# Kernel tuning notes

Hardware: AMD Instinct MI355X
Metric: run time of the kernel (lower is better)

The kernel has to match this reference:

```python
import jax, jax.numpy as jnp
import numpy as np

D = 12  # grid size per axis (self.shape = [12,12,12])
BN_EPS = 1e-5


def _scatter(feats, idx, B):
    # feats: [N, C], idx: [N, 4] = (b, z, y, x). Coords are unique -> .set is exact.
    g = jnp.zeros((B, D, D, D, feats.shape[-1]), feats.dtype)
    return g.at[idx[:, 0], idx[:, 1], idx[:, 2], idx[:, 3]].set(feats)


def _subm_conv_bn_relu(feats, idx, B, W, b, gamma, beta):
    # Submanifold 3x3x3 conv == dense SAME conv on zero-filled grid, restricted
    # to the active sites (inactive neighbors contribute zero features).
    g = _scatter(feats, idx, B)  # [B, D, D, D, Cin]
    y = jax.lax.conv_general_dilated(
        g, W, window_strides=(1, 1, 1), padding='SAME',
        dimension_numbers=('NDHWC', 'DHWIO', 'NDHWC')) + b
    f = y[idx[:, 0], idx[:, 1], idx[:, 2], idx[:, 3]]  # gather active -> [N, Cout]
    # BatchNorm1d (training mode): biased batch stats over the N active points.
    mu = f.mean(axis=0)
    var = f.var(axis=0)
    f = (f - mu) * jax.lax.rsqrt(var + BN_EPS) * gamma + beta
    return jax.nn.relu(f)


def setup_inputs() -> dict:
    key = jax.random.key(0)
    B, per, Cin = 512, 864, 16
    N = B * per
    k_feat, k_coord, kp = jax.random.split(key, 3)
    # unique active voxels per batch element
    pkeys = jax.random.split(k_coord, B)
    lin = jax.vmap(lambda k: jax.random.permutation(k, D * D * D))(pkeys)[:, :per]  # [B, per]
    z, y, x = lin // (D * D), (lin // D) % D, lin % D
    bids = jnp.broadcast_to(jnp.arange(B)[:, None], (B, per))
    indices = jnp.stack([bids, z, y, x], axis=-1).reshape(N, 4).astype(jnp.int32)
    features = jax.random.normal(k_feat, (N, Cin), dtype=jnp.float32)
    ks = jax.random.split(kp, 6)
    inp = {
        'features': features, 'indices': indices, 'batch_size': B,
        'W0': jax.random.normal(ks[0], (3, 3, 3, Cin, 64), jnp.float32) * 0.05,
        'b0': jax.random.normal(ks[1], (64,), jnp.float32) * 0.05,
        'gamma0': jnp.ones((64,), jnp.float32), 'beta0': jnp.zeros((64,), jnp.float32),
        'W1': jax.random.normal(ks[2], (3, 3, 3, 64, 128), jnp.float32) * 0.05,
        'b1': jax.random.normal(ks[3], (128,), jnp.float32) * 0.05,
        'gamma1': jnp.ones((128,), jnp.float32), 'beta1': jnp.zeros((128,), jnp.float32),
        'W2': jax.random.normal(ks[4], (3, 3, 3, 128, 64), jnp.float32) * 0.05,
        'b2': jax.random.normal(ks[5], (64,), jnp.float32) * 0.05,
        'gamma2': jnp.ones((64,), jnp.float32), 'beta2': jnp.zeros((64,), jnp.float32),
    }
    return inp


def reference(features, indices, batch_size, W0, b0, gamma0, beta0,
              W1, b1, gamma1, beta1, W2, b2, gamma2, beta2):
    B = int(batch_size)
    f = _subm_conv_bn_relu(features, indices, B, W0, b0, gamma0, beta0)
    f = _subm_conv_bn_relu(f, indices, B, W1, b1, gamma1, beta1)
    f = _subm_conv_bn_relu(f, indices, B, W2, b2, gamma2, beta2)
    g = _scatter(f, indices, B)                 # [B, D, D, D, Cout]
    return jnp.transpose(g, (0, 4, 1, 2, 3))    # spconv .dense(): [B, C, D, H, W]
```

## Files before the change

### kernel.cpp

```cpp
#include <hip/hip_runtime.h>

#define DD 12
#define VOX 1728
#define BN_EPS 1e-5f
#define BATCH 512
#define PER 864
#define PERZ 865

typedef __attribute__((ext_vector_type(8))) short short8;
typedef __attribute__((ext_vector_type(4))) float f32x4;
typedef unsigned short u16;

__device__ inline u16 f2b(float f) {
    union { float f; unsigned u; } v; v.f = f;
    unsigned r = v.u + 0x7fffu + ((v.u >> 16) & 1u);
    return (u16)(r >> 16);
}
__device__ inline float b2f(u16 h) {
    union { unsigned u; float f; } v; v.u = ((unsigned)h) << 16;
    return v.f;
}
constexpr int ilog2(int v) { return v == 1 ? 0 : 1 + ilog2(v / 2); }

__device__ __forceinline__ void async_copy16(const void* g, void* l) {
    __builtin_amdgcn_global_load_lds(
        (const __attribute__((address_space(1))) void*)g,
        (__attribute__((address_space(3))) void*)l, 16, 0, 0);
}

template<int N> __device__ __forceinline__ void wait_vm() {
    if constexpr (N == 0)       asm volatile("s_waitcnt vmcnt(0)"  ::: "memory");
    else if constexpr (N == 8)  asm volatile("s_waitcnt vmcnt(8)"  ::: "memory");
    else if constexpr (N == 10) asm volatile("s_waitcnt vmcnt(10)" ::: "memory");
    else if constexpr (N == 12) asm volatile("s_waitcnt vmcnt(12)" ::: "memory");
    else if constexpr (N == 18) asm volatile("s_waitcnt vmcnt(18)" ::: "memory");
    else static_assert(N == 0, "unhandled vmcnt value");
}

__global__ void build_map_kernel(const int* __restrict__ idx, int* __restrict__ map, int N) {
    int p = blockIdx.x * blockDim.x + threadIdx.x;
    if (p >= N) return;
    const int4 v = ((const int4*)idx)[p];
    map[v.x * VOX + (v.y * DD + v.z) * DD + v.w] = p;
}

__global__ void build_nbr_kernel(const int* __restrict__ idx, const int* __restrict__ map,
                                 u16* __restrict__ nbr, int N) {
    int t = blockIdx.x * blockDim.x + threadIdx.x;
    int p = t >> 5, nk = t & 31;
    if (p >= N) return;
    u16 out = PER;
    if (nk < 27) {
        const int4 v = ((const int4*)idx)[p];
        int dz = nk / 9 - 1, dy = (nk / 3) % 3 - 1, dx = nk % 3 - 1;
        int zz = v.y + dz, yy = v.z + dy, xx = v.w + dx;
        if (zz >= 0 && zz < DD && yy >= 0 && yy < DD && xx >= 0 && xx < DD) {
            int q = map[v.x * VOX + (zz * DD + yy) * DD + xx];
            if (q >= 0) out = (u16)(q - v.x * PER);
        }
    }
    nbr[t] = out;
}

__global__ void transpose_w_kernel(const float* __restrict__ W, u16* __restrict__ Wt,
                                   int K, int COUT, int Kpad) {
    int i = blockIdx.x * blockDim.x + threadIdx.x;
    if (i >= K * COUT) return;
    int n = i % COUT, k = i / COUT;
    Wt[(size_t)n * Kpad + k] = f2b(W[i]);
}

__global__ void zero_rows_kernel(u16* __restrict__ f, int CIN) {
    int t = blockIdx.x * blockDim.x + threadIdx.x;
    int e4 = CIN >> 2;
    if (t >= BATCH * e4) return;
    int b = t / e4, k = t - b * e4;
    ((ushort4*)f)[(size_t)(b * PERZ + PER) * e4 + k] = make_ushort4(0, 0, 0, 0);
}

__global__ void cast_bf16_kernel(const float* __restrict__ in, u16* __restrict__ out, int N4) {
    int i = blockIdx.x * blockDim.x + threadIdx.x;
    if (i >= N4) return;
    float4 v = ((const float4*)in)[i];
    int p = i >> 2, c4 = i & 3;
    int b = p / PER, r = p - b * PER;
    ushort4 o;
    o.x = f2b(v.x); o.y = f2b(v.y); o.z = f2b(v.z); o.w = f2b(v.w);
    ((ushort4*)out)[(size_t)(b * PERZ + r) * 4 + c4] = o;
}

template<int CIN, int COUT, int BM, int WM, int WN>
__global__ __launch_bounds__(256) void conv_mfma_kernel(
    const u16* __restrict__ fin,
    const u16* __restrict__ nbr,
    const u16* __restrict__ Wt,
    const float* __restrict__ bias,
    float* __restrict__ y,
    float* __restrict__ stats) {
    constexpr int Kpad   = (27 * CIN + 63) & ~63;
    constexpr int KSTEPS = Kpad / 64;
    constexpr int L2C    = ilog2(CIN);
    constexpr int BN     = WN * 64;
    constexpr int ASLOTS = BM / 32;
    constexpr int BSLOTS = BN / 32;
    constexpr int A_OFF  = BN * 128;
    constexpr int BUFB   = (BM + BN) * 128;
    static_assert(KSTEPS >= 3, "pipeline prologue needs >=3 K-steps");
    __shared__ char smem[2 * BUFB];

    const int perx = gridDim.x >> 3;
    const int bid = (blockIdx.x & 7) * perx + (blockIdx.x >> 3);
    const int p0 = bid * BM;

    const int tid = threadIdx.x;
    const int wave = tid >> 6, lane = tid & 63;
    const int wm = wave / WN, wn = wave % WN;
    const int lq = lane >> 4, lr = lane & 15;
    const int lrow = lane >> 3;
    const int kc_d = (lane & 7) ^ (lrow & 7);

    int qvoff[ASLOTS], gbase[ASLOTS];
    #pragma unroll
    for (int i = 0; i < ASLOTS; i++) {
        int m = (wave * ASLOTS + i) * 8 + lrow;
        int p = p0 + m;
        int b = p / PER;
        qvoff[i] = p * 64 + (((kc_d * 8) >> L2C) * 2);
        gbase[i] = b * PERZ * CIN + ((kc_d * 8) & (CIN - 1));
    }
    int bvoff[BSLOTS];
    #pragma unroll
    for (int j = 0; j < BSLOTS; j++)
        bvoff[j] = ((wave * BSLOTS + j) * 8 + lrow) * Kpad + kc_d * 8;

    int phs[2];
    phs[0] = ((0 + lq) ^ (lr & 7)) * 16;
    phs[1] = ((4 + lq) ^ (lr & 7)) * 16;
    const int aBase = A_OFF + (wm * 64 + lr) * 128;
    const int bBase = (wn * 64 + lr) * 128;

    const f32x4 fzero = {0.f, 0.f, 0.f, 0.f};
    f32x4 acc[4][4];
    #pragma unroll
    for (int i = 0; i < 4; i++)
        #pragma unroll
        for (int j = 0; j < 4; j++) acc[i][j] = fzero;

    u16 q[ASLOTS];
    auto loadQ = [&](int step) {
        int sQ = ((step * 64) >> L2C) * 2;
        #pragma unroll
        for (int i = 0; i < ASLOTS; i++)
            q[i] = *(const u16*)((const char*)nbr + qvoff[i] + sQ);
    };
    auto stage = [&](int step, int bo) {
        int sG = (step * 64) & (CIN - 1);
        const u16* fs = fin + sG;
        #pragma unroll
        for (int i = 0; i < ASLOTS; i++)
            async_copy16(fs + gbase[i] + ((int)q[i] << L2C),
                         smem + bo + A_OFF + (wave * ASLOTS + i) * 1024);
        const u16* wsrc = Wt + step * 64;
        #pragma unroll
        for (int j = 0; j < BSLOTS; j++)
            async_copy16(wsrc + bvoff[j], smem + bo + (wave * BSLOTS + j) * 1024);
    };

    loadQ(0);
    stage(0, 0);
    loadQ(1);

    #pragma unroll 1
    for (int kb = 0; kb < KSTEPS; kb++) {
        if (kb + 1 < KSTEPS) {
            stage(kb + 1, ((kb + 1) & 1) * BUFB);
            if (kb + 2 < KSTEPS) {
                loadQ(kb + 2);
                wait_vm<2 * ASLOTS + BSLOTS>();
            } else {
                wait_vm<ASLOTS + BSLOTS>();
            }
        } else {
            wait_vm<0>();
        }
        __builtin_amdgcn_s_barrier();

        const int so = (kb & 1) * BUFB;
        #pragma unroll
        for (int s = 0; s < 2; s++) {
            short8 af[4], bfr[4];
            #pragma unroll
            for (int i = 0; i < 4; i++)
                af[i] = *(const short8*)(smem + so + aBase + i * 2048 + phs[s]);
            #pragma unroll
            for (int j = 0; j < 4; j++)
                bfr[j] = *(const short8*)(smem + so + bBase + j * 2048 + phs[s]);
            #pragma unroll
            for (int i = 0; i < 4; i++)
                #pragma unroll
                for (int j = 0; j < 4; j++)
                    acc[i][j] = __builtin_amdgcn_mfma_f32_16x16x32_bf16(af[i], bfr[j], acc[i][j], 0, 0, 0);
        }
        asm volatile("s_waitcnt lgkmcnt(0)" ::: "memory");
        __builtin_amdgcn_s_barrier();
    }

    #pragma unroll
    for (int j = 0; j < 4; j++) {
        int col = wn * 64 + j * 16 + lr;
        float bv = bias[col];
        float s = 0.f, s2 = 0.f;
        #pragma unroll
        for (int i = 0; i < 4; i++) {
            int row0 = p0 + wm * 64 + i * 16 + lq * 4;
            #pragma unroll
            for (int r = 0; r < 4; r++) {
                float v = acc[i][j][r] + bv;
                y[(size_t)(row0 + r) * COUT + col] = v;
                s += v; s2 += v * v;
            }
        }
        s  += __shfl_down(s, 32);  s  += __shfl_down(s, 16);
        s2 += __shfl_down(s2, 32); s2 += __shfl_down(s2, 16);
        if (lane < 16) {
            atomicAdd(&stats[col], s);
            atomicAdd(&stats[COUT + col], s2);
        }
    }
}

template<int COUT>
__global__ void finalize_kernel(const float* __restrict__ stats, const float* __restrict__ gamma,
                                const float* __restrict__ beta, float* __restrict__ ss, int N) {
    int co = threadIdx.x;
    float inv_n = 1.f / (float)N;
    float mu  = stats[co] * inv_n;
    float var = stats[COUT + co] * inv_n - mu * mu;
    float sc  = gamma[co] * rsqrtf(var + BN_EPS);
    ss[co]        = sc;
    ss[COUT + co] = beta[co] - mu * sc;
}

template<int COUT>
__global__ void apply_kernel(const float* __restrict__ y, const float* __restrict__ ss,
                             u16* __restrict__ f, int total4) {
    int i = blockIdx.x * blockDim.x + threadIdx.x;
    if (i >= total4) return;
    constexpr int E4 = COUT / 4;
    float4 v = ((const float4*)y)[i];
    int p = i / E4, k = i - p * E4;
    int c0 = k * 4;
    int b = p / PER, r = p - b * PER;
    ushort4 o;
    float a;
    a = fmaf(v.x, ss[c0 + 0], ss[COUT + c0 + 0]); o.x = f2b(a > 0.f ? a : 0.f);
    a = fmaf(v.y, ss[c0 + 1], ss[COUT + c0 + 1]); o.y = f2b(a > 0.f ? a : 0.f);
    a = fmaf(v.z, ss[c0 + 2], ss[COUT + c0 + 2]); o.z = f2b(a > 0.f ? a : 0.f);
    a = fmaf(v.w, ss[c0 + 3], ss[COUT + c0 + 3]); o.w = f2b(a > 0.f ? a : 0.f);
    ((ushort4*)f)[(size_t)(b * PERZ + r) * E4 + k] = o;
}

__global__ void output_kernel(const u16* __restrict__ f, const int* __restrict__ map,
                              float* __restrict__ out, int total) {
    int i = blockIdx.x * blockDim.x + threadIdx.x;
    if (i >= total) return;
    int voxel = i % VOX;
    int bc    = i / VOX;
    int c = bc & 63;
    int b = bc >> 6;
    int p = map[b * VOX + voxel];
    float v = 0.f;
    if (p >= 0) {
        int r = p - b * PER;
        v = b2f(f[(size_t)(b * PERZ + r) * 64 + c]);
    }
    out[i] = v;
}

extern "C" void kernel_launch(void* const* d_in, const int* in_sizes, int n_in,
                              void* d_out, int out_size, void* d_ws, size_t ws_size,
                              hipStream_t stream) {
    const float* feats = (const float*)d_in[0];
    const int*   idx   = (const int*)  d_in[1];
    const float* W0 = (const float*)d_in[3];
    const float* b0 = (const float*)d_in[4];
    const float* g0 = (const float*)d_in[5];
    const float* e0 = (const float*)d_in[6];
    const float* W1 = (const float*)d_in[7];
    const float* b1 = (const float*)d_in[8];
    const float* g1 = (const float*)d_in[9];
    const float* e1 = (const float*)d_in[10];
    const float* W2 = (const float*)d_in[11];
    const float* b2 = (const float*)d_in[12];
    const float* g2 = (const float*)d_in[13];
    const float* e2 = (const float*)d_in[14];

    const int N = in_sizes[0] / 16;

    char* ws = (char*)d_ws;
    size_t off = 0;
    auto alloc = [&](size_t bytes) { void* p = ws + off; off = (off + bytes + 255) & ~(size_t)255; return p; };
    int*   map   = (int*)  alloc((size_t)BATCH * VOX * 4);
    float* stats = (float*)alloc(3 * 256 * 4);
    float* ss    = (float*)alloc(3 * 256 * 4);
    u16*   nbr   = (u16*)  alloc((size_t)N * 32 * 2);
    u16*   wt0   = (u16*)  alloc((size_t)64  * 448  * 2);
    u16*   wt1   = (u16*)  alloc((size_t)128 * 1728 * 2);
    u16*   wt2   = (u16*)  alloc((size_t)64  * 3456 * 2);
    u16*   fbuf  = (u16*)  alloc((size_t)BATCH * PERZ * 128 * 2);
    float* y = (float*)d_out;

    hipMemsetAsync(map,   0xFF, (size_t)BATCH * VOX * 4, stream);
    hipMemsetAsync(stats, 0,    3 * 256 * 4, stream);
    hipMemsetAsync(wt0,   0,    (size_t)64 * 448 * 2, stream);
    build_map_kernel<<<(N + 255) / 256, 256, 0, stream>>>(idx, map, N);
    build_nbr_kernel<<<(N * 32 + 255) / 256, 256, 0, stream>>>(idx, map, nbr, N);
    transpose_w_kernel<<<(432  * 64  + 255) / 256, 256, 0, stream>>>(W0, wt0, 432,  64,  448);
    transpose_w_kernel<<<(1728 * 128 + 255) / 256, 256, 0, stream>>>(W1, wt1, 1728, 128, 1728);
    transpose_w_kernel<<<(3456 * 64  + 255) / 256, 256, 0, stream>>>(W2, wt2, 3456, 64,  3456);

    zero_rows_kernel<<<(BATCH * 4 + 255) / 256, 256, 0, stream>>>(fbuf, 16);
    cast_bf16_kernel<<<(N * 4 + 255) / 256, 256, 0, stream>>>(feats, fbuf, N * 4);
    conv_mfma_kernel<16, 64, 256, 4, 1><<<N / 256, 256, 0, stream>>>(fbuf, nbr, wt0, b0, y, stats + 0);
    finalize_kernel<64><<<1, 64, 0, stream>>>(stats + 0, g0, e0, ss + 0, N);
    zero_rows_kernel<<<(BATCH * 16 + 255) / 256, 256, 0, stream>>>(fbuf, 64);
    apply_kernel<64><<<(N * 16 + 255) / 256, 256, 0, stream>>>(y, ss + 0, fbuf, N * 16);

    conv_mfma_kernel<64, 128, 128, 2, 2><<<N / 128, 256, 0, stream>>>(fbuf, nbr, wt1, b1, y, stats + 256);
    finalize_kernel<128><<<1, 128, 0, stream>>>(stats + 256, g1, e1, ss + 256, N);
    zero_rows_kernel<<<(BATCH * 32 + 255) / 256, 256, 0, stream>>>(fbuf, 128);
    apply_kernel<128><<<(N * 32 + 255) / 256, 256, 0, stream>>>(y, ss + 256, fbuf, N * 32);

    conv_mfma_kernel<128, 64, 256, 4, 1><<<N / 256, 256, 0, stream>>>(fbuf, nbr, wt2, b2, y, stats + 512);
    finalize_kernel<64><<<1, 64, 0, stream>>>(stats + 512, g2, e2, ss + 512, N);
    zero_rows_kernel<<<(BATCH * 16 + 255) / 256, 256, 0, stream>>>(fbuf, 64);
    apply_kernel<64><<<(N * 16 + 255) / 256, 256, 0, stream>>>(y, ss + 512, fbuf, N * 16);

    output_kernel<<<(out_size + 255) / 256, 256, 0, stream>>>(fbuf, map, (float*)d_out, out_size);
}
```

Measured before the change: 1.389 ms.

## Gather A-operand fragments directly into registers instead of staging through LDS

The conv MFMA kernel no longer stages the gathered neighbor features (A operand) in shared memory. Each lane loads its MFMA A fragments straight from global memory into registers, double-buffered across K-steps, while only the weights (B) still go through LDS with async copies. This removes the A-tile LDS round trip and shrinks shared memory per block, which may raise occupancy. In exchange it adds register pressure and uncoalesced per-lane 16-byte global loads, and the vmcnt wait counts become more complex.

```diff
diff --git a/kernel.cpp b/kernel.cpp
--- a/kernel.cpp
+++ b/kernel.cpp
@@ -30,9 +30,10 @@
 
 template<int N> __device__ __forceinline__ void wait_vm() {
     if constexpr (N == 0)       asm volatile("s_waitcnt vmcnt(0)"  ::: "memory");
-    else if constexpr (N == 8)  asm volatile("s_waitcnt vmcnt(8)"  ::: "memory");
     else if constexpr (N == 10) asm volatile("s_waitcnt vmcnt(10)" ::: "memory");
     else if constexpr (N == 12) asm volatile("s_waitcnt vmcnt(12)" ::: "memory");
+    else if constexpr (N == 14) asm volatile("s_waitcnt vmcnt(14)" ::: "memory");
+    else if constexpr (N == 16) asm volatile("s_waitcnt vmcnt(16)" ::: "memory");
     else if constexpr (N == 18) asm volatile("s_waitcnt vmcnt(18)" ::: "memory");
     else static_assert(N == 0, "unhandled vmcnt value");
 }
@@ -99,12 +100,11 @@
     float* __restrict__ stats) {
     constexpr int Kpad   = (27 * CIN + 63) & ~63;
     constexpr int KSTEPS = Kpad / 64;
-    constexpr int L2C    = ilog2(CIN);
     constexpr int BN     = WN * 64;
-    constexpr int ASLOTS = BM / 32;
     constexpr int BSLOTS = BN / 32;
-    constexpr int A_OFF  = BN * 128;
-    constexpr int BUFB   = (BM + BN) * 128;
+    constexpr int NS     = (CIN == 16) ? 2 : 1;
+    constexpr int NQ     = 4 * NS;
+    constexpr int BUFB   = BN * 128;
     static_assert(KSTEPS >= 3, "pipeline prologue needs >=3 K-steps");
     __shared__ char smem[2 * BUFB];
 
@@ -119,15 +119,6 @@
     const int lrow = lane >> 3;
     const int kc_d = (lane & 7) ^ (lrow & 7);
 
-    int qvoff[ASLOTS], gbase[ASLOTS];
-    #pragma unroll
-    for (int i = 0; i < ASLOTS; i++) {
-        int m = (wave * ASLOTS + i) * 8 + lrow;
-        int p = p0 + m;
-        int b = p / PER;
-        qvoff[i] = p * 64 + (((kc_d * 8) >> L2C) * 2);
-        gbase[i] = b * PERZ * CIN + ((kc_d * 8) & (CIN - 1));
-    }
     int bvoff[BSLOTS];
     #pragma unroll
     for (int j = 0; j < BSLOTS; j++)
@@ -136,8 +127,18 @@
     int phs[2];
     phs[0] = ((0 + lq) ^ (lr & 7)) * 16;
     phs[1] = ((4 + lq) ^ (lr & 7)) * 16;
-    const int aBase = A_OFF + (wm * 64 + lr) * 128;
     const int bBase = (wn * 64 + lr) * 128;
+
+    const char* nbrB = (const char*)nbr;
+    const char* finB = (const char*)fin;
+    int nbq[4], abase[4];
+    #pragma unroll
+    for (int i = 0; i < 4; i++) {
+        int p = p0 + wm * 64 + i * 16 + lr;
+        int b = p / PER;
+        nbq[i]   = p * 64;
+        abase[i] = b * PERZ * CIN * 2;
+    }
 
     const f32x4 fzero = {0.f, 0.f, 0.f, 0.f};
     f32x4 acc[4][4];
@@ -146,63 +147,86 @@
         #pragma unroll
         for (int j = 0; j < 4; j++) acc[i][j] = fzero;
 
-    u16 q[ASLOTS];
-    auto loadQ = [&](int step) {
-        int sQ = ((step * 64) >> L2C) * 2;
-        #pragma unroll
-        for (int i = 0; i < ASLOTS; i++)
-            q[i] = *(const u16*)((const char*)nbr + qvoff[i] + sQ);
-    };
-    auto stage = [&](int step, int bo) {
-        int sG = (step * 64) & (CIN - 1);
-        const u16* fs = fin + sG;
-        #pragma unroll
-        for (int i = 0; i < ASLOTS; i++)
-            async_copy16(fs + gbase[i] + ((int)q[i] << L2C),
-                         smem + bo + A_OFF + (wave * ASLOTS + i) * 1024);
-        const u16* wsrc = Wt + step * 64;
+    u16 qX[4][NS], qY[4][NS];
+    short8 aX[8], aY[8];
+
+    auto loadQ = [&](int s, u16 (&qq)[4][NS]) {
+        #pragma unroll
+        for (int i = 0; i < 4; i++)
+            #pragma unroll
+            for (int ns = 0; ns < NS; ns++) {
+                int tap;
+                if constexpr (CIN == 16)       tap = s * 4 + ns * 2 + (lq >> 1);
+                else if constexpr (CIN == 64)  tap = s;
+                else                           tap = s >> 1;
+                qq[i][ns] = *(const u16*)(nbrB + nbq[i] + tap * 2);
+            }
+    };
+    auto issueA = [&](int s, short8 (&aa)[8], u16 (&qq)[4][NS]) {
+        #pragma unroll
+        for (int i = 0; i < 4; i++)
+            #pragma unroll
+            for (int sh = 0; sh < 2; sh++) {
+                int ch;
+                if constexpr (CIN == 16)       ch = (lq & 1) * 8;
+                else if constexpr (CIN == 64)  ch = sh * 32 + lq * 8;
+                else                           ch = (s & 1) * 64 + sh * 32 + lq * 8;
+                int q = (NS == 2) ? (int)qq[i][sh] : (int)qq[i][0];
+                aa[i * 2 + sh] = *(const short8*)(finB + abase[i] + q * (CIN * 2) + ch * 2);
+            }
+    };
+    auto stageB = [&](int s, int so) {
+        const u16* wsrc = Wt + s * 64;
         #pragma unroll
         for (int j = 0; j < BSLOTS; j++)
-            async_copy16(wsrc + bvoff[j], smem + bo + (wave * BSLOTS + j) * 1024);
-    };
-
-    loadQ(0);
-    stage(0, 0);
-    loadQ(1);
-
-    #pragma unroll 1
-    for (int kb = 0; kb < KSTEPS; kb++) {
-        if (kb + 1 < KSTEPS) {
-            stage(kb + 1, ((kb + 1) & 1) * BUFB);
-            if (kb + 2 < KSTEPS) {
-                loadQ(kb + 2);
-                wait_vm<2 * ASLOTS + BSLOTS>();
-            } else {
-                wait_vm<ASLOTS + BSLOTS>();
-            }
-        } else {
-            wait_vm<0>();
-        }
-        __builtin_amdgcn_s_barrier();
-
-        const int so = (kb & 1) * BUFB;
-        #pragma unroll
-        for (int s = 0; s < 2; s++) {
-            short8 af[4], bfr[4];
-            #pragma unroll
-            for (int i = 0; i < 4; i++)
-                af[i] = *(const short8*)(smem + so + aBase + i * 2048 + phs[s]);
+            async_copy16(wsrc + bvoff[j], smem + so + (wave * BSLOTS + j) * 1024);
+    };
+    auto compute = [&](short8 (&aa)[8], int so) {
+        #pragma unroll
+        for (int sh = 0; sh < 2; sh++) {
+            short8 bfr[4];
             #pragma unroll
             for (int j = 0; j < 4; j++)
-                bfr[j] = *(const short8*)(smem + so + bBase + j * 2048 + phs[s]);
+                bfr[j] = *(const short8*)(smem + so + bBase + j * 2048 + phs[sh]);
             #pragma unroll
             for (int i = 0; i < 4; i++)
                 #pragma unroll
                 for (int j = 0; j < 4; j++)
-                    acc[i][j] = __builtin_amdgcn_mfma_f32_16x16x32_bf16(af[i], bfr[j], acc[i][j], 0, 0, 0);
-        }
+                    acc[i][j] = __builtin_amdgcn_mfma_f32_16x16x32_bf16(aa[i * 2 + sh], bfr[j], acc[i][j], 0, 0, 0);
+        }
+    };
+
+    auto step_body = [&](int k, short8 (&aC)[8], short8 (&aN)[8],
+                         u16 (&qI)[4][NS], u16 (&qL)[4][NS], int soC, int soN) {
+        const bool haveNext = (k + 1 < KSTEPS);
+        const bool haveQ    = (k + 2 < KSTEPS);
+        if (haveNext) {
+            stageB(k + 1, soN);
+            issueA(k + 1, aN, qI);
+        }
+        if (haveQ) loadQ(k + 2, qL);
+        if (haveNext) {
+            if (haveQ) wait_vm<BSLOTS + 8 + NQ>();
+            else       wait_vm<BSLOTS + 8>();
+        } else {
+            wait_vm<0>();
+        }
+        __builtin_amdgcn_s_barrier();
+        compute(aC, soC);
         asm volatile("s_waitcnt lgkmcnt(0)" ::: "memory");
         __builtin_amdgcn_s_barrier();
+    };
+
+    loadQ(0, qX);
+    issueA(0, aX, qX);
+    stageB(0, 0);
+    loadQ(1, qY);
+
+    #pragma unroll 1
+    for (int kb = 0; kb < KSTEPS; kb += 2) {
+        step_body(kb, aX, aY, qY, qX, 0, BUFB);
+        if (kb + 1 < KSTEPS)
+            step_body(kb + 1, aY, aX, qX, qY, BUFB, 0);
     }
 
     #pragma unroll
```

After: 2.093 ms. 50.7% more time.
